# Kernel optimization log

Hardware: AMD Instinct MI355X
Metric: run time of the kernel (lower is better)

Reference implementation:

```python
import jax, jax.numpy as jnp
import numpy as np

B = 1024      # molecules (segments)
K = 16        # conformers per molecule
N = B * K     # total nodes
C = 128       # in_out_dimension
HID = 256     # hidden_dimension of gate MLP
HEADS = 2
LAYERS = 2


def _leaky(x, slope):
    return jnp.where(x >= 0, x, slope * x)


def setup_inputs() -> dict:
    key = jax.random.key(0)
    ks = jax.random.split(key, 12)
    # segment ids: K conformers per molecule, sorted
    batch = jnp.repeat(jnp.arange(B, dtype=jnp.int64), K)
    # fully connected within each segment, no self loops, then append self loops
    idx = np.arange(N, dtype=np.int64).reshape(B, K)
    src = np.broadcast_to(idx[:, :, None], (B, K, K)).reshape(-1)
    dst = np.broadcast_to(idx[:, None, :], (B, K, K)).reshape(-1)
    keep = src != dst
    e_src = jnp.asarray(np.concatenate([src[keep], np.arange(N, dtype=np.int64)]))
    e_dst = jnp.asarray(np.concatenate([dst[keep], np.arange(N, dtype=np.int64)]))
    sc = 1.0 / np.sqrt(C)
    sh = 1.0 / np.sqrt(HID)
    inp = {
        "H": jax.random.normal(ks[0], (N, C), jnp.float32),
        "batch": batch,
        "edge_src": e_src,
        "edge_dst": e_dst,
        "Wl": jax.random.normal(ks[1], (LAYERS, C, HEADS * C), jnp.float32) * sc,
        "bl": jnp.zeros((LAYERS, HEADS * C), jnp.float32),
        "Wr": jax.random.normal(ks[2], (LAYERS, C, HEADS * C), jnp.float32) * sc,
        "br": jnp.zeros((LAYERS, HEADS * C), jnp.float32),
        "att": jax.random.normal(ks[3], (LAYERS, HEADS, C), jnp.float32) * sc,
        "gat_bias": jnp.zeros((LAYERS, C), jnp.float32),
        "gW1": jax.random.normal(ks[4], (C, HID), jnp.float32) * sc,
        "gb1": jnp.zeros((HID,), jnp.float32),
        "gW2": jax.random.normal(ks[5], (HID, HID), jnp.float32) * sh,
        "gb2": jnp.zeros((HID,), jnp.float32),
        "gW3": jax.random.normal(ks[6], (HID, 1), jnp.float32) * sh,
        "gb3": jnp.zeros((1,), jnp.float32),
    }
    return inp


def _segment_softmax(logits, seg, num_segments):
    m = jax.ops.segment_max(logits, seg, num_segments=num_segments)
    ex = jnp.exp(logits - m[seg])
    den = jax.ops.segment_sum(ex, seg, num_segments=num_segments)
    return ex / den[seg]


def _gatv2(x, e_src, e_dst, Wl, bl, Wr, br, att, bias):
    # GATv2Conv, concat=False (mean over heads), negative_slope=0.2
    xl = (x @ Wl + bl).reshape(N, HEADS, C)   # source transform
    xr = (x @ Wr + br).reshape(N, HEADS, C)   # target transform
    e = _leaky(xl[e_src] + xr[e_dst], 0.2)    # [E, H, C]
    logits = jnp.einsum('ehc,hc->eh', e, att) # [E, H]
    alpha = _segment_softmax(logits, e_dst, N)
    out = jax.ops.segment_sum(xl[e_src] * alpha[:, :, None], e_dst, num_segments=N)
    return out.mean(axis=1) + bias            # [N, C]


def reference(H, batch, edge_src, edge_dst, Wl, bl, Wr, br, att, gat_bias,
              gW1, gb1, gW2, gb2, gW3, gb3):
    x = H
    for l in range(LAYERS):
        x = _gatv2(x, edge_src, edge_dst, Wl[l], bl[l], Wr[l], br[l], att[l], gat_bias[l])
    # gate MLP (LeakyReLU default slope 0.01)
    h = _leaky(x @ gW1 + gb1, 0.01)
    h = _leaky(h @ gW2 + gb2, 0.01)
    h_gate = h @ gW3 + gb3                    # [N, 1]
    scores = _segment_softmax(h_gate, batch, B)
    h_pool = jax.ops.segment_sum(x * scores, batch, num_segments=B)  # [B, C]
    return (h_pool, scores)
```

## Files before the change

kernel.cpp:

```cpp
#include <hip/hip_runtime.h>
#include <hip/hip_bf16.h>
#include <math.h>

#define N_NODES 16384
#define B_MOL   1024

typedef __attribute__((ext_vector_type(8))) short short8v;
typedef __attribute__((ext_vector_type(4))) float f32x4;

static __device__ __forceinline__ unsigned short f2bf(float f) {
    unsigned int u = __float_as_uint(f);
    unsigned int r = (u + 0x7FFFu + ((u >> 16) & 1u)) >> 16;
    return (unsigned short)r;
}
static __device__ __forceinline__ float bf2f(unsigned short h) {
    return __uint_as_float(((unsigned int)h) << 16);
}

__global__ __launch_bounds__(256)
void conv_pack(const float* __restrict__ Wl, const float* __restrict__ Wr,
               const float* __restrict__ g1, const float* __restrict__ g2,
               unsigned short* __restrict__ wpk) {
    int idx = blockIdx.x * 256 + threadIdx.x;
    if (idx >= 229376) return;
    float v; size_t base; int nK, k, col;
    if (idx < 131072) {
        int l = idx >> 16;
        int e = idx & 65535;
        k = e >> 9; col = e & 511;
        v = (col < 256) ? Wl[l * 32768 + k * 256 + col]
                        : Wr[l * 32768 + k * 256 + (col - 256)];
        base = (size_t)l * 131072; nK = 4;
    } else if (idx < 163840) {
        int e = idx - 131072; k = e >> 8; col = e & 255;
        v = g1[k * 256 + col]; base = 262144; nK = 4;
    } else {
        int e = idx - 163840; k = e >> 8; col = e & 255;
        v = g2[k * 256 + col]; base = 327680; nK = 8;
    }
    int cb = col >> 4, ci = col & 15, ks = k >> 5, kk = k & 31;
    int lane = ((kk >> 3) << 4) | ci;
    size_t fo = ((size_t)(cb * nK + ks) * 2) * 512 + lane * 8 + (kk & 7);
    unsigned short h = f2bf(v);
    wpk[base + fo] = h;
    wpk[base + fo + 512] = f2bf(v - bf2f(h));
}

template<int NK, int NCB>
static __device__ __forceinline__ void tile_gemm(
        const short* __restrict__ Ah, const short* __restrict__ Al,
        const unsigned short* __restrict__ wv,
        f32x4 (&acc)[2][NCB], int lane) {
    int lr = lane & 15;
    int kq = (lane >> 4) * 8;
    short8v bc[NCB][2], bn[NCB][2];
    #pragma unroll
    for (int j = 0; j < NCB; ++j) {
        bc[j][0] = *(const short8v*)&wv[((j * NK + 0) * 2 + 0) * 512 + lane * 8];
        bc[j][1] = *(const short8v*)&wv[((j * NK + 0) * 2 + 1) * 512 + lane * 8];
    }
    #pragma unroll
    for (int ks = 0; ks < NK; ++ks) {
        if (ks + 1 < NK) {
            #pragma unroll
            for (int j = 0; j < NCB; ++j) {
                bn[j][0] = *(const short8v*)&wv[((j * NK + ks + 1) * 2 + 0) * 512 + lane * 8];
                bn[j][1] = *(const short8v*)&wv[((j * NK + ks + 1) * 2 + 1) * 512 + lane * 8];
            }
        }
        short8v ah[2], al[2];
        #pragma unroll
        for (int i = 0; i < 2; ++i) {
            int ro = (i * 16 + lr) * 264 + ks * 32 + kq;
            ah[i] = *(const short8v*)&Ah[ro];
            al[i] = *(const short8v*)&Al[ro];
        }
        #pragma unroll
        for (int i = 0; i < 2; ++i)
            #pragma unroll
            for (int j = 0; j < NCB; ++j) {
                acc[i][j] = __builtin_amdgcn_mfma_f32_16x16x32_bf16(ah[i], bc[j][0], acc[i][j], 0, 0, 0);
                acc[i][j] = __builtin_amdgcn_mfma_f32_16x16x32_bf16(ah[i], bc[j][1], acc[i][j], 0, 0, 0);
                acc[i][j] = __builtin_amdgcn_mfma_f32_16x16x32_bf16(al[i], bc[j][0], acc[i][j], 0, 0, 0);
            }
        if (ks + 1 < NK) {
            #pragma unroll
            for (int j = 0; j < NCB; ++j) { bc[j][0] = bn[j][0]; bc[j][1] = bn[j][1]; }
        }
    }
}

static __device__ __forceinline__ void pack_pair(f32x4 o, short4* ph, short4* pl) {
    unsigned short h0 = f2bf(o[0]), h1 = f2bf(o[1]), h2 = f2bf(o[2]), h3 = f2bf(o[3]);
    *ph = make_short4((short)h0, (short)h1, (short)h2, (short)h3);
    *pl = make_short4((short)f2bf(o[0] - bf2f(h0)), (short)f2bf(o[1] - bf2f(h1)),
                      (short)f2bf(o[2] - bf2f(h2)), (short)f2bf(o[3] - bf2f(h3)));
}

__global__ __launch_bounds__(512, 1)
void mega(const float* __restrict__ H, const unsigned short* __restrict__ wpk,
          const float* __restrict__ bl, const float* __restrict__ br,
          const float* __restrict__ att, const float* __restrict__ gbias,
          const float* __restrict__ gb1, const float* __restrict__ gb2,
          const float* __restrict__ gW3, const float* __restrict__ gb3,
          float* __restrict__ out) {
    __shared__ short sAh[32][264], sAl[32][264];
    __shared__ float sL[32][260], sR[32][260];
    __shared__ float sXf[32][132];
    __shared__ float sLog[2][32][20];
    __shared__ float sg[32], ssc[32];

    int tid  = threadIdx.x;
    int lane = tid & 63;
    int w    = tid >> 6;
    int lr   = lane & 15;
    int rowBase = blockIdx.x * 32;

    {
        int r = tid >> 4, q = tid & 15;
        const float* hp = H + (size_t)(rowBase + r) * 128 + q * 8;
        #pragma unroll
        for (int u = 0; u < 2; ++u) {
            f32x4 v = *(const f32x4*)&hp[u * 4];
            pack_pair(v, (short4*)&sAh[r][q * 8 + u * 4], (short4*)&sAl[r][q * 8 + u * 4]);
        }
    }
    __syncthreads();

    for (int l = 0; l < 2; ++l) {
        {
            f32x4 acc[2][4];
            #pragma unroll
            for (int i = 0; i < 2; ++i)
                #pragma unroll
                for (int j = 0; j < 4; ++j) acc[i][j] = (f32x4){0.f, 0.f, 0.f, 0.f};
            tile_gemm<4, 4>(&sAh[0][0], &sAl[0][0],
                            wpk + (size_t)l * 131072 + (size_t)w * 16384, acc, lane);
            float* dst; int cbase; const float* bp;
            if (w < 4) { dst = &sL[0][0]; cbase = w * 64; bp = bl + l * 256 + w * 64; }
            else       { dst = &sR[0][0]; cbase = (w - 4) * 64; bp = br + l * 256 + (w - 4) * 64; }
            #pragma unroll
            for (int i = 0; i < 2; ++i) {
                int row0 = i * 16 + (lane >> 4) * 4;
                #pragma unroll
                for (int j = 0; j < 4; ++j) {
                    int cl = j * 16 + lr;
                    float bv = bp[cl];
                    #pragma unroll
                    for (int t = 0; t < 4; ++t)
                        dst[(row0 + t) * 260 + cbase + cl] = acc[i][j][t] + bv;
                }
            }
        }
        __syncthreads();

        {
            int m2l = tid >> 8;
            int r8  = tid & 255;
            int hh  = r8 >> 7;
            int db  = (r8 >> 5) & 3;
            int sb  = (r8 >> 3) & 3;
            int cq  = r8 & 7;
            float ac[4][4];
            #pragma unroll
            for (int di = 0; di < 4; ++di)
                #pragma unroll
                for (int si = 0; si < 4; ++si) ac[di][si] = 0.f;
            #pragma unroll
            for (int t = 0; t < 4; ++t) {
                int c4 = cq + 8 * t;
                f32x4 av = *(const f32x4*)&att[l * 256 + hh * 128 + c4 * 4];
                f32x4 a6 = av * 0.6f, a4 = av * 0.4f;
                f32x4 xrv[4], xlv[4];
                #pragma unroll
                for (int di = 0; di < 4; ++di)
                    xrv[di] = *(const f32x4*)&sR[m2l * 16 + db * 4 + di][hh * 128 + c4 * 4];
                #pragma unroll
                for (int si = 0; si < 4; ++si)
                    xlv[si] = *(const f32x4*)&sL[m2l * 16 + sb * 4 + si][hh * 128 + c4 * 4];
                #pragma unroll
                for (int di = 0; di < 4; ++di)
                    #pragma unroll
                    for (int si = 0; si < 4; ++si) {
                        f32x4 e = xlv[si] + xrv[di];
                        ac[di][si] += a6[0] * e[0] + a4[0] * fabsf(e[0])
                                    + a6[1] * e[1] + a4[1] * fabsf(e[1])
                                    + a6[2] * e[2] + a4[2] * fabsf(e[2])
                                    + a6[3] * e[3] + a4[3] * fabsf(e[3]);
                    }
            }
            #pragma unroll
            for (int di = 0; di < 4; ++di)
                #pragma unroll
                for (int si = 0; si < 4; ++si) {
                    float v = ac[di][si];
                    v += __shfl_down(v, 4);
                    v += __shfl_down(v, 2);
                    v += __shfl_down(v, 1);
                    if (cq == 0)
                        sLog[m2l][(db * 4 + di) * 2 + hh][sb * 4 + si] = v;
                }
        }
        __syncthreads();

        if (tid < 64) {
            int ms = tid >> 5, dhs = tid & 31;
            float vb[16], mx = -1e30f;
            #pragma unroll
            for (int s = 0; s < 16; ++s) { vb[s] = sLog[ms][dhs][s]; mx = fmaxf(mx, vb[s]); }
            float den = 0.f;
            #pragma unroll
            for (int s = 0; s < 16; ++s) { vb[s] = expf(vb[s] - mx); den += vb[s]; }
            float inv = 1.f / den;
            #pragma unroll
            for (int s = 0; s < 16; ++s) sLog[ms][dhs][s] = vb[s] * inv;
        }
        __syncthreads();

        {
            int m2a = tid >> 8;
            int d  = (tid >> 4) & 15;
            int cw = tid & 15;
            f32x4 f0 = (f32x4){0.f, 0.f, 0.f, 0.f};
            f32x4 f1 = (f32x4){0.f, 0.f, 0.f, 0.f};
            #pragma unroll
            for (int hh = 0; hh < 2; ++hh) {
                const float* alr = &sLog[m2a][d * 2 + hh][0];
                #pragma unroll
                for (int s = 0; s < 16; ++s) {
                    int se = (s + cw) & 15;
                    float al = alr[se];
                    const float* xp = &sL[m2a * 16 + se][hh * 128 + cw * 8];
                    f0 += al * *(const f32x4*)xp;
                    f1 += al * *(const f32x4*)(xp + 4);
                }
            }
            f32x4 o0 = f0 * 0.5f + *(const f32x4*)&gbias[l * 128 + cw * 8];
            f32x4 o1 = f1 * 0.5f + *(const f32x4*)&gbias[l * 128 + cw * 8 + 4];
            int row = m2a * 16 + d;
            pack_pair(o0, (short4*)&sAh[row][cw * 8],     (short4*)&sAl[row][cw * 8]);
            pack_pair(o1, (short4*)&sAh[row][cw * 8 + 4], (short4*)&sAl[row][cw * 8 + 4]);
            if (l == 1) {
                *(f32x4*)&sXf[row][cw * 8]     = o0;
                *(f32x4*)&sXf[row][cw * 8 + 4] = o1;
            }
        }
        __syncthreads();
    }

    {
        f32x4 acc[2][2];
        #pragma unroll
        for (int i = 0; i < 2; ++i)
            #pragma unroll
            for (int j = 0; j < 2; ++j) acc[i][j] = (f32x4){0.f, 0.f, 0.f, 0.f};
        tile_gemm<4, 2>(&sAh[0][0], &sAl[0][0],
                        wpk + 262144 + (size_t)w * 8192, acc, lane);
        __syncthreads();
        #pragma unroll
        for (int i = 0; i < 2; ++i) {
            int row0 = i * 16 + (lane >> 4) * 4;
            #pragma unroll
            for (int j = 0; j < 2; ++j) {
                int cl = w * 32 + j * 16 + lr;
                float bv = gb1[cl];
                #pragma unroll
                for (int t = 0; t < 4; ++t) {
                    float v = acc[i][j][t] + bv;
                    v = v >= 0.f ? v : 0.01f * v;
                    unsigned short h = f2bf(v);
                    sAh[row0 + t][cl] = (short)h;
                    sAl[row0 + t][cl] = (short)f2bf(v - bf2f(h));
                }
            }
        }
    }
    __syncthreads();

    {
        f32x4 acc[2][2];
        #pragma unroll
        for (int i = 0; i < 2; ++i)
            #pragma unroll
            for (int j = 0; j < 2; ++j) acc[i][j] = (f32x4){0.f, 0.f, 0.f, 0.f};
        tile_gemm<8, 2>(&sAh[0][0], &sAl[0][0],
                        wpk + 327680 + (size_t)w * 16384, acc, lane);
        #pragma unroll
        for (int i = 0; i < 2; ++i) {
            int row0 = i * 16 + (lane >> 4) * 4;
            #pragma unroll
            for (int j = 0; j < 2; ++j) {
                int cl = w * 32 + j * 16 + lr;
                float bv = gb2[cl];
                #pragma unroll
                for (int t = 0; t < 4; ++t) {
                    float v = acc[i][j][t] + bv;
                    v = v >= 0.f ? v : 0.01f * v;
                    sR[row0 + t][cl] = v;
                }
            }
        }
    }
    __syncthreads();

    {
        int grow = tid >> 4, l16 = tid & 15;
        float p = 0.f;
        #pragma unroll
        for (int u = 0; u < 4; ++u) {
            f32x4 h2v = *(const f32x4*)&sR[grow][l16 * 16 + u * 4];
            f32x4 w3v = *(const f32x4*)&gW3[l16 * 16 + u * 4];
            p += h2v[0] * w3v[0] + h2v[1] * w3v[1] + h2v[2] * w3v[2] + h2v[3] * w3v[3];
        }
        p += __shfl_down(p, 8);
        p += __shfl_down(p, 4);
        p += __shfl_down(p, 2);
        p += __shfl_down(p, 1);
        if (l16 == 0) sg[grow] = p + gb3[0];
    }
    __syncthreads();

    if (tid < 32) {
        float v = sg[tid];
        float mx = v;
        #pragma unroll
        for (int off = 8; off; off >>= 1) mx = fmaxf(mx, __shfl_xor(mx, off, 16));
        float e = expf(v - mx);
        float den = e;
        #pragma unroll
        for (int off = 8; off; off >>= 1) den += __shfl_xor(den, off, 16);
        float sc = e / den;
        ssc[tid] = sc;
        out[131072 + rowBase + tid] = sc;
    }
    __syncthreads();

    if (tid < 256) {
        int cc = tid & 127;
        int mp = tid >> 7;
        float a = 0.f;
        #pragma unroll
        for (int s = 0; s < 16; ++s)
            a += ssc[mp * 16 + s] * sXf[mp * 16 + s][cc];
        out[(size_t)(blockIdx.x * 2 + mp) * 128 + cc] = a;
    }
}

extern "C" void kernel_launch(void* const* d_in, const int* in_sizes, int n_in,
                              void* d_out, int out_size, void* d_ws, size_t ws_size,
                              hipStream_t stream) {
    (void)in_sizes; (void)n_in; (void)out_size; (void)ws_size;
    const float* H        = (const float*)d_in[0];
    const float* Wl       = (const float*)d_in[4];
    const float* bl       = (const float*)d_in[5];
    const float* Wr       = (const float*)d_in[6];
    const float* br       = (const float*)d_in[7];
    const float* att      = (const float*)d_in[8];
    const float* gat_bias = (const float*)d_in[9];
    const float* gW1      = (const float*)d_in[10];
    const float* gb1      = (const float*)d_in[11];
    const float* gW2      = (const float*)d_in[12];
    const float* gb2      = (const float*)d_in[13];
    const float* gW3      = (const float*)d_in[14];
    const float* gb3      = (const float*)d_in[15];
    float* out = (float*)d_out;

    unsigned short* wpk = (unsigned short*)d_ws;

    conv_pack<<<896, 256, 0, stream>>>(Wl, Wr, gW1, gW2, wpk);
    mega<<<512, 512, 0, stream>>>(H, wpk, bl, br, att, gat_bias,
                                  gb1, gb2, gW3, gb3, out);
}
```

Before: 65.89 us.

## Remap mega kernel to one molecule per 256-thread block

Each block now handles a single 16-node molecule with 4 waves instead of two molecules with 8 waves, doubling the grid to 1024 blocks. Shared memory is roughly halved and launch bounds target 3 blocks per CU, so more blocks can be resident and overlap their barrier-separated phases. The GEMM helper now works on one 16-row tile with MFMAs grouped by weight fragment, and each wave covers twice the output columns. The trade-off is that weights are read from global memory by twice as many blocks, and each block does less work per barrier.

```diff
diff --git a/kernel.cpp b/kernel.cpp
--- a/kernel.cpp
+++ b/kernel.cpp
@@ -47,10 +47,10 @@
 }
 
 template<int NK, int NCB>
-static __device__ __forceinline__ void tile_gemm(
+static __device__ __forceinline__ void tile_gemm16(
         const short* __restrict__ Ah, const short* __restrict__ Al,
         const unsigned short* __restrict__ wv,
-        f32x4 (&acc)[2][NCB], int lane) {
+        f32x4 (&acc)[NCB], int lane) {
     int lr = lane & 15;
     int kq = (lane >> 4) * 8;
     short8v bc[NCB][2], bn[NCB][2];
@@ -68,21 +68,18 @@
                 bn[j][1] = *(const short8v*)&wv[((j * NK + ks + 1) * 2 + 1) * 512 + lane * 8];
             }
         }
-        short8v ah[2], al[2];
-        #pragma unroll
-        for (int i = 0; i < 2; ++i) {
-            int ro = (i * 16 + lr) * 264 + ks * 32 + kq;
-            ah[i] = *(const short8v*)&Ah[ro];
-            al[i] = *(const short8v*)&Al[ro];
-        }
-        #pragma unroll
-        for (int i = 0; i < 2; ++i)
-            #pragma unroll
-            for (int j = 0; j < NCB; ++j) {
-                acc[i][j] = __builtin_amdgcn_mfma_f32_16x16x32_bf16(ah[i], bc[j][0], acc[i][j], 0, 0, 0);
-                acc[i][j] = __builtin_amdgcn_mfma_f32_16x16x32_bf16(ah[i], bc[j][1], acc[i][j], 0, 0, 0);
-                acc[i][j] = __builtin_amdgcn_mfma_f32_16x16x32_bf16(al[i], bc[j][0], acc[i][j], 0, 0, 0);
-            }
+        int ro = lr * 264 + ks * 32 + kq;
+        short8v ah = *(const short8v*)&Ah[ro];
+        short8v al = *(const short8v*)&Al[ro];
+        #pragma unroll
+        for (int j = 0; j < NCB; ++j)
+            acc[j] = __builtin_amdgcn_mfma_f32_16x16x32_bf16(ah, bc[j][0], acc[j], 0, 0, 0);
+        #pragma unroll
+        for (int j = 0; j < NCB; ++j)
+            acc[j] = __builtin_amdgcn_mfma_f32_16x16x32_bf16(ah, bc[j][1], acc[j], 0, 0, 0);
+        #pragma unroll
+        for (int j = 0; j < NCB; ++j)
+            acc[j] = __builtin_amdgcn_mfma_f32_16x16x32_bf16(al, bc[j][0], acc[j], 0, 0, 0);
         if (ks + 1 < NK) {
             #pragma unroll
             for (int j = 0; j < NCB; ++j) { bc[j][0] = bn[j][0]; bc[j][1] = bn[j][1]; }
@@ -97,24 +94,24 @@
                       (short)f2bf(o[2] - bf2f(h2)), (short)f2bf(o[3] - bf2f(h3)));
 }
 
-__global__ __launch_bounds__(512, 1)
+__global__ __launch_bounds__(256, 3)
 void mega(const float* __restrict__ H, const unsigned short* __restrict__ wpk,
           const float* __restrict__ bl, const float* __restrict__ br,
           const float* __restrict__ att, const float* __restrict__ gbias,
           const float* __restrict__ gb1, const float* __restrict__ gb2,
           const float* __restrict__ gW3, const float* __restrict__ gb3,
           float* __restrict__ out) {
-    __shared__ short sAh[32][264], sAl[32][264];
-    __shared__ float sL[32][260], sR[32][260];
-    __shared__ float sXf[32][132];
-    __shared__ float sLog[2][32][20];
-    __shared__ float sg[32], ssc[32];
+    __shared__ short sAh[16][264], sAl[16][264];
+    __shared__ float sL[16][260], sR[16][260];
+    __shared__ float sLog[32][20];
+    __shared__ float sg[16], ssc[16];
 
     int tid  = threadIdx.x;
     int lane = tid & 63;
     int w    = tid >> 6;
     int lr   = lane & 15;
-    int rowBase = blockIdx.x * 32;
+    int mol  = blockIdx.x;
+    int rowBase = mol * 16;
 
     {
         int r = tid >> 4, q = tid & 15;
@@ -128,39 +125,34 @@
     __syncthreads();
 
     for (int l = 0; l < 2; ++l) {
+        #pragma unroll
+        for (int c = 0; c < 2; ++c) {
+            f32x4 acc[4];
+            #pragma unroll
+            for (int j = 0; j < 4; ++j) acc[j] = (f32x4){0.f, 0.f, 0.f, 0.f};
+            tile_gemm16<4, 4>(&sAh[0][0], &sAl[0][0],
+                              wpk + (size_t)l * 131072 + ((size_t)w * 8 + c * 4) * 4096,
+                              acc, lane);
+            float* dst; int cbase; const float* bp;
+            if (w < 2) { dst = &sL[0][0]; cbase = w * 128 + c * 64; bp = bl + l * 256; }
+            else       { dst = &sR[0][0]; cbase = (w - 2) * 128 + c * 64; bp = br + l * 256; }
+            int row0 = (lane >> 4) * 4;
+            #pragma unroll
+            for (int j = 0; j < 4; ++j) {
+                int cl = cbase + j * 16 + lr;
+                float bv = bp[cl];
+                #pragma unroll
+                for (int t = 0; t < 4; ++t)
+                    dst[(row0 + t) * 260 + cl] = acc[j][t] + bv;
+            }
+        }
+        __syncthreads();
+
         {
-            f32x4 acc[2][4];
-            #pragma unroll
-            for (int i = 0; i < 2; ++i)
-                #pragma unroll
-                for (int j = 0; j < 4; ++j) acc[i][j] = (f32x4){0.f, 0.f, 0.f, 0.f};
-            tile_gemm<4, 4>(&sAh[0][0], &sAl[0][0],
-                            wpk + (size_t)l * 131072 + (size_t)w * 16384, acc, lane);
-            float* dst; int cbase; const float* bp;
-            if (w < 4) { dst = &sL[0][0]; cbase = w * 64; bp = bl + l * 256 + w * 64; }
-            else       { dst = &sR[0][0]; cbase = (w - 4) * 64; bp = br + l * 256 + (w - 4) * 64; }
-            #pragma unroll
-            for (int i = 0; i < 2; ++i) {
-                int row0 = i * 16 + (lane >> 4) * 4;
-                #pragma unroll
-                for (int j = 0; j < 4; ++j) {
-                    int cl = j * 16 + lr;
-                    float bv = bp[cl];
-                    #pragma unroll
-                    for (int t = 0; t < 4; ++t)
-                        dst[(row0 + t) * 260 + cbase + cl] = acc[i][j][t] + bv;
-                }
-            }
-        }
-        __syncthreads();
-
-        {
-            int m2l = tid >> 8;
-            int r8  = tid & 255;
-            int hh  = r8 >> 7;
-            int db  = (r8 >> 5) & 3;
-            int sb  = (r8 >> 3) & 3;
-            int cq  = r8 & 7;
+            int hh  = tid >> 7;
+            int db  = (tid >> 5) & 3;
+            int sb  = (tid >> 3) & 3;
+            int cq  = tid & 7;
             float ac[4][4];
             #pragma unroll
             for (int di = 0; di < 4; ++di)
@@ -174,10 +166,10 @@
                 f32x4 xrv[4], xlv[4];
                 #pragma unroll
                 for (int di = 0; di < 4; ++di)
-                    xrv[di] = *(const f32x4*)&sR[m2l * 16 + db * 4 + di][hh * 128 + c4 * 4];
+                    xrv[di] = *(const f32x4*)&sR[db * 4 + di][hh * 128 + c4 * 4];
                 #pragma unroll
                 for (int si = 0; si < 4; ++si)
-                    xlv[si] = *(const f32x4*)&sL[m2l * 16 + sb * 4 + si][hh * 128 + c4 * 4];
+                    xlv[si] = *(const f32x4*)&sL[sb * 4 + si][hh * 128 + c4 * 4];
                 #pragma unroll
                 for (int di = 0; di < 4; ++di)
                     #pragma unroll
@@ -198,106 +190,93 @@
                     v += __shfl_down(v, 2);
                     v += __shfl_down(v, 1);
                     if (cq == 0)
-                        sLog[m2l][(db * 4 + di) * 2 + hh][sb * 4 + si] = v;
+                        sLog[(db * 4 + di) * 2 + hh][sb * 4 + si] = v;
                 }
         }
         __syncthreads();
 
-        if (tid < 64) {
-            int ms = tid >> 5, dhs = tid & 31;
+        if (tid < 32) {
             float vb[16], mx = -1e30f;
             #pragma unroll
-            for (int s = 0; s < 16; ++s) { vb[s] = sLog[ms][dhs][s]; mx = fmaxf(mx, vb[s]); }
+            for (int s = 0; s < 16; ++s) { vb[s] = sLog[tid][s]; mx = fmaxf(mx, vb[s]); }
             float den = 0.f;
             #pragma unroll
             for (int s = 0; s < 16; ++s) { vb[s] = expf(vb[s] - mx); den += vb[s]; }
             float inv = 1.f / den;
             #pragma unroll
-            for (int s = 0; s < 16; ++s) sLog[ms][dhs][s] = vb[s] * inv;
+            for (int s = 0; s < 16; ++s) sLog[tid][s] = vb[s] * inv;
         }
         __syncthreads();
 
         {
-            int m2a = tid >> 8;
-            int d  = (tid >> 4) & 15;
+            int d  = tid >> 4;
             int cw = tid & 15;
             f32x4 f0 = (f32x4){0.f, 0.f, 0.f, 0.f};
             f32x4 f1 = (f32x4){0.f, 0.f, 0.f, 0.f};
             #pragma unroll
             for (int hh = 0; hh < 2; ++hh) {
-                const float* alr = &sLog[m2a][d * 2 + hh][0];
+                const float* alr = &sLog[d * 2 + hh][0];
                 #pragma unroll
                 for (int s = 0; s < 16; ++s) {
                     int se = (s + cw) & 15;
                     float al = alr[se];
-                    const float* xp = &sL[m2a * 16 + se][hh * 128 + cw * 8];
+                    const float* xp = &sL[se][hh * 128 + cw * 8];
                     f0 += al * *(const f32x4*)xp;
                     f1 += al * *(const f32x4*)(xp + 4);
                 }
             }
             f32x4 o0 = f0 * 0.5f + *(const f32x4*)&gbias[l * 128 + cw * 8];
             f32x4 o1 = f1 * 0.5f + *(const f32x4*)&gbias[l * 128 + cw * 8 + 4];
-            int row = m2a * 16 + d;
-            pack_pair(o0, (short4*)&sAh[row][cw * 8],     (short4*)&sAl[row][cw * 8]);
-            pack_pair(o1, (short4*)&sAh[row][cw * 8 + 4], (short4*)&sAl[row][cw * 8 + 4]);
+            pack_pair(o0, (short4*)&sAh[d][cw * 8],     (short4*)&sAl[d][cw * 8]);
+            pack_pair(o1, (short4*)&sAh[d][cw * 8 + 4], (short4*)&sAl[d][cw * 8 + 4]);
             if (l == 1) {
-                *(f32x4*)&sXf[row][cw * 8]     = o0;
-                *(f32x4*)&sXf[row][cw * 8 + 4] = o1;
+                *(f32x4*)&sR[d][128 + cw * 8]     = o0;
+                *(f32x4*)&sR[d][128 + cw * 8 + 4] = o1;
             }
         }
         __syncthreads();
     }
 
     {
-        f32x4 acc[2][2];
-        #pragma unroll
-        for (int i = 0; i < 2; ++i)
-            #pragma unroll
-            for (int j = 0; j < 2; ++j) acc[i][j] = (f32x4){0.f, 0.f, 0.f, 0.f};
-        tile_gemm<4, 2>(&sAh[0][0], &sAl[0][0],
-                        wpk + 262144 + (size_t)w * 8192, acc, lane);
-        __syncthreads();
-        #pragma unroll
-        for (int i = 0; i < 2; ++i) {
-            int row0 = i * 16 + (lane >> 4) * 4;
-            #pragma unroll
-            for (int j = 0; j < 2; ++j) {
-                int cl = w * 32 + j * 16 + lr;
-                float bv = gb1[cl];
-                #pragma unroll
-                for (int t = 0; t < 4; ++t) {
-                    float v = acc[i][j][t] + bv;
-                    v = v >= 0.f ? v : 0.01f * v;
-                    unsigned short h = f2bf(v);
-                    sAh[row0 + t][cl] = (short)h;
-                    sAl[row0 + t][cl] = (short)f2bf(v - bf2f(h));
-                }
+        f32x4 acc[4];
+        #pragma unroll
+        for (int j = 0; j < 4; ++j) acc[j] = (f32x4){0.f, 0.f, 0.f, 0.f};
+        tile_gemm16<4, 4>(&sAh[0][0], &sAl[0][0],
+                          wpk + 262144 + (size_t)w * 16384, acc, lane);
+        __syncthreads();
+        int row0 = (lane >> 4) * 4;
+        #pragma unroll
+        for (int j = 0; j < 4; ++j) {
+            int cl = w * 64 + j * 16 + lr;
+            float bv = gb1[cl];
+            #pragma unroll
+            for (int t = 0; t < 4; ++t) {
+                float v = acc[j][t] + bv;
+                v = v >= 0.f ? v : 0.01f * v;
+                unsigned short h = f2bf(v);
+                sAh[row0 + t][cl] = (short)h;
+                sAl[row0 + t][cl] = (short)f2bf(v - bf2f(h));
             }
         }
     }
     __syncthreads();
 
     {
-        f32x4 acc[2][2];
-        #pragma unroll
-        for (int i = 0; i < 2; ++i)
-            #pragma unroll
-            for (int j = 0; j < 2; ++j) acc[i][j] = (f32x4){0.f, 0.f, 0.f, 0.f};
-        tile_gemm<8, 2>(&sAh[0][0], &sAl[0][0],
-                        wpk + 327680 + (size_t)w * 16384, acc, lane);
-        #pragma unroll
-        for (int i = 0; i < 2; ++i) {
-            int row0 = i * 16 + (lane >> 4) * 4;
-            #pragma unroll
-            for (int j = 0; j < 2; ++j) {
-                int cl = w * 32 + j * 16 + lr;
-                float bv = gb2[cl];
-                #pragma unroll
-                for (int t = 0; t < 4; ++t) {
-                    float v = acc[i][j][t] + bv;
-                    v = v >= 0.f ? v : 0.01f * v;
-                    sR[row0 + t][cl] = v;
-                }
+        f32x4 acc[4];
+        #pragma unroll
+        for (int j = 0; j < 4; ++j) acc[j] = (f32x4){0.f, 0.f, 0.f, 0.f};
+        tile_gemm16<8, 4>(&sAh[0][0], &sAl[0][0],
+                          wpk + 327680 + (size_t)w * 32768, acc, lane);
+        int row0 = (lane >> 4) * 4;
+        #pragma unroll
+        for (int j = 0; j < 4; ++j) {
+            int cl = w * 64 + j * 16 + lr;
+            float bv = gb2[cl];
+            #pragma unroll
+            for (int t = 0; t < 4; ++t) {
+                float v = acc[j][t] + bv;
+                v = v >= 0.f ? v : 0.01f * v;
+                sL[row0 + t][cl] = v;
             }
         }
     }
@@ -308,7 +287,7 @@
         float p = 0.f;
         #pragma unroll
         for (int u = 0; u < 4; ++u) {
-            f32x4 h2v = *(const f32x4*)&sR[grow][l16 * 16 + u * 4];
+            f32x4 h2v = *(const f32x4*)&sL[grow][l16 * 16 + u * 4];
             f32x4 w3v = *(const f32x4*)&gW3[l16 * 16 + u * 4];
             p += h2v[0] * w3v[0] + h2v[1] * w3v[1] + h2v[2] * w3v[2] + h2v[3] * w3v[3];
         }
@@ -320,7 +299,7 @@
     }
     __syncthreads();
 
-    if (tid < 32) {
+    if (tid < 16) {
         float v = sg[tid];
         float mx = v;
         #pragma unroll
@@ -335,14 +314,12 @@
     }
     __syncthreads();
 
-    if (tid < 256) {
-        int cc = tid & 127;
-        int mp = tid >> 7;
+    if (tid < 128) {
         float a = 0.f;
         #pragma unroll
         for (int s = 0; s < 16; ++s)
-            a += ssc[mp * 16 + s] * sXf[mp * 16 + s][cc];
-        out[(size_t)(blockIdx.x * 2 + mp) * 128 + cc] = a;
+            a += ssc[s] * sR[s][128 + tid];
+        out[(size_t)mol * 128 + tid] = a;
     }
 }
 
@@ -368,6 +345,6 @@
     unsigned short* wpk = (unsigned short*)d_ws;
 
     conv_pack<<<896, 256, 0, stream>>>(Wl, Wr, gW1, gW2, wpk);
-    mega<<<512, 512, 0, stream>>>(H, wpk, bl, br, att, gat_bias,
-                                  gb1, gb2, gW3, gb3, out);
-}
+    mega<<<B_MOL, 256, 0, stream>>>(H, wpk, bl, br, att, gat_bias,
+                                    gb1, gb2, gW3, gb3, out);
+}
```

After: 107.4 us. 62.9% more time.

## Double block threads to 1024 and split GEMM and attention work finer

Applied to the files above, without the earlier changes.

Each block now runs 1024 threads (16 waves) instead of 512 over the same 32-row tile. Each wave gets half as many column blocks in every GEMM. The attention logits are computed one (dst, head, src) pair per thread with the segment softmax fused in via shuffles, which removes a separate softmax pass and one barrier. The att vector is staged in shared memory, and the sXf buffer is dropped by reusing sR. This raises in-block parallelism and latency hiding, but each wave does less MFMA work per weight load and register pressure per thread is capped tighter.

```diff
diff --git a/kernel.cpp b/kernel.cpp
--- a/kernel.cpp
+++ b/kernel.cpp
@@ -47,7 +47,7 @@
 }
 
 template<int NK, int NCB>
-static __device__ __forceinline__ void tile_gemm(
+static __device__ __forceinline__ void tile_gemm32(
         const short* __restrict__ Ah, const short* __restrict__ Al,
         const unsigned short* __restrict__ wv,
         f32x4 (&acc)[2][NCB], int lane) {
@@ -97,7 +97,7 @@
                       (short)f2bf(o[2] - bf2f(h2)), (short)f2bf(o[3] - bf2f(h3)));
 }
 
-__global__ __launch_bounds__(512, 1)
+__global__ __launch_bounds__(1024)
 void mega(const float* __restrict__ H, const unsigned short* __restrict__ wpk,
           const float* __restrict__ bl, const float* __restrict__ br,
           const float* __restrict__ att, const float* __restrict__ gbias,
@@ -106,8 +106,8 @@
           float* __restrict__ out) {
     __shared__ short sAh[32][264], sAl[32][264];
     __shared__ float sL[32][260], sR[32][260];
-    __shared__ float sXf[32][132];
     __shared__ float sLog[2][32][20];
+    __shared__ float sAtt[512];
     __shared__ float sg[32], ssc[32];
 
     int tid  = threadIdx.x;
@@ -117,206 +117,154 @@
     int rowBase = blockIdx.x * 32;
 
     {
-        int r = tid >> 4, q = tid & 15;
-        const float* hp = H + (size_t)(rowBase + r) * 128 + q * 8;
-        #pragma unroll
-        for (int u = 0; u < 2; ++u) {
-            f32x4 v = *(const f32x4*)&hp[u * 4];
-            pack_pair(v, (short4*)&sAh[r][q * 8 + u * 4], (short4*)&sAl[r][q * 8 + u * 4]);
-        }
+        int r = tid >> 5, q = tid & 31;
+        f32x4 v = *(const f32x4*)&H[(size_t)(rowBase + r) * 128 + q * 4];
+        pack_pair(v, (short4*)&sAh[r][q * 4], (short4*)&sAl[r][q * 4]);
+        if (tid < 512) sAtt[tid] = att[tid];
     }
     __syncthreads();
 
     for (int l = 0; l < 2; ++l) {
         {
-            f32x4 acc[2][4];
+            f32x4 acc[2][2];
             #pragma unroll
             for (int i = 0; i < 2; ++i)
                 #pragma unroll
-                for (int j = 0; j < 4; ++j) acc[i][j] = (f32x4){0.f, 0.f, 0.f, 0.f};
-            tile_gemm<4, 4>(&sAh[0][0], &sAl[0][0],
-                            wpk + (size_t)l * 131072 + (size_t)w * 16384, acc, lane);
+                for (int j = 0; j < 2; ++j) acc[i][j] = (f32x4){0.f, 0.f, 0.f, 0.f};
+            tile_gemm32<4, 2>(&sAh[0][0], &sAl[0][0],
+                              wpk + (size_t)l * 131072 + (size_t)w * 8192, acc, lane);
             float* dst; int cbase; const float* bp;
-            if (w < 4) { dst = &sL[0][0]; cbase = w * 64; bp = bl + l * 256 + w * 64; }
-            else       { dst = &sR[0][0]; cbase = (w - 4) * 64; bp = br + l * 256 + (w - 4) * 64; }
+            if (w < 8) { dst = &sL[0][0]; cbase = w * 32; bp = bl + l * 256; }
+            else       { dst = &sR[0][0]; cbase = (w - 8) * 32; bp = br + l * 256; }
             #pragma unroll
             for (int i = 0; i < 2; ++i) {
                 int row0 = i * 16 + (lane >> 4) * 4;
                 #pragma unroll
-                for (int j = 0; j < 4; ++j) {
-                    int cl = j * 16 + lr;
+                for (int j = 0; j < 2; ++j) {
+                    int cl = cbase + j * 16 + lr;
                     float bv = bp[cl];
                     #pragma unroll
                     for (int t = 0; t < 4; ++t)
-                        dst[(row0 + t) * 260 + cbase + cl] = acc[i][j][t] + bv;
+                        dst[(row0 + t) * 260 + cl] = acc[i][j][t] + bv;
                 }
             }
         }
         __syncthreads();
 
         {
-            int m2l = tid >> 8;
-            int r8  = tid & 255;
-            int hh  = r8 >> 7;
-            int db  = (r8 >> 5) & 3;
-            int sb  = (r8 >> 3) & 3;
-            int cq  = r8 & 7;
-            float ac[4][4];
-            #pragma unroll
-            for (int di = 0; di < 4; ++di)
-                #pragma unroll
-                for (int si = 0; si < 4; ++si) ac[di][si] = 0.f;
-            #pragma unroll
-            for (int t = 0; t < 4; ++t) {
-                int c4 = cq + 8 * t;
-                f32x4 av = *(const f32x4*)&att[l * 256 + hh * 128 + c4 * 4];
-                f32x4 a6 = av * 0.6f, a4 = av * 0.4f;
-                f32x4 xrv[4], xlv[4];
-                #pragma unroll
-                for (int di = 0; di < 4; ++di)
-                    xrv[di] = *(const f32x4*)&sR[m2l * 16 + db * 4 + di][hh * 128 + c4 * 4];
-                #pragma unroll
-                for (int si = 0; si < 4; ++si)
-                    xlv[si] = *(const f32x4*)&sL[m2l * 16 + sb * 4 + si][hh * 128 + c4 * 4];
-                #pragma unroll
-                for (int di = 0; di < 4; ++di)
-                    #pragma unroll
-                    for (int si = 0; si < 4; ++si) {
-                        f32x4 e = xlv[si] + xrv[di];
-                        ac[di][si] += a6[0] * e[0] + a4[0] * fabsf(e[0])
-                                    + a6[1] * e[1] + a4[1] * fabsf(e[1])
-                                    + a6[2] * e[2] + a4[2] * fabsf(e[2])
-                                    + a6[3] * e[3] + a4[3] * fabsf(e[3]);
-                    }
-            }
-            #pragma unroll
-            for (int di = 0; di < 4; ++di)
-                #pragma unroll
-                for (int si = 0; si < 4; ++si) {
-                    float v = ac[di][si];
-                    v += __shfl_down(v, 4);
-                    v += __shfl_down(v, 2);
-                    v += __shfl_down(v, 1);
-                    if (cq == 0)
-                        sLog[m2l][(db * 4 + di) * 2 + hh][sb * 4 + si] = v;
-                }
+            int m2l = tid >> 9;
+            int rem = tid & 511;
+            int dh  = rem >> 4;
+            int s   = rem & 15;
+            int d   = dh >> 1, hh = dh & 1;
+            const float* xrp = &sR[m2l * 16 + d][hh * 128];
+            const float* xlp = &sL[m2l * 16 + s][hh * 128];
+            const float* ap  = &sAtt[l * 256 + hh * 128];
+            float ac = 0.f;
+            #pragma unroll 8
+            for (int c4 = 0; c4 < 32; ++c4) {
+                f32x4 av = *(const f32x4*)&ap[c4 * 4];
+                f32x4 xv = *(const f32x4*)&xlp[c4 * 4];
+                f32x4 rv = *(const f32x4*)&xrp[c4 * 4];
+                f32x4 e = xv + rv;
+                ac += 0.6f * av[0] * e[0] + 0.4f * av[0] * fabsf(e[0])
+                    + 0.6f * av[1] * e[1] + 0.4f * av[1] * fabsf(e[1])
+                    + 0.6f * av[2] * e[2] + 0.4f * av[2] * fabsf(e[2])
+                    + 0.6f * av[3] * e[3] + 0.4f * av[3] * fabsf(e[3]);
+            }
+            float mx = ac;
+            #pragma unroll
+            for (int off = 1; off < 16; off <<= 1)
+                mx = fmaxf(mx, __shfl_xor(mx, off, 16));
+            float e = expf(ac - mx);
+            float den = e;
+            #pragma unroll
+            for (int off = 1; off < 16; off <<= 1)
+                den += __shfl_xor(den, off, 16);
+            sLog[m2l][dh][s] = e / den;
         }
         __syncthreads();
 
-        if (tid < 64) {
-            int ms = tid >> 5, dhs = tid & 31;
-            float vb[16], mx = -1e30f;
-            #pragma unroll
-            for (int s = 0; s < 16; ++s) { vb[s] = sLog[ms][dhs][s]; mx = fmaxf(mx, vb[s]); }
-            float den = 0.f;
-            #pragma unroll
-            for (int s = 0; s < 16; ++s) { vb[s] = expf(vb[s] - mx); den += vb[s]; }
-            float inv = 1.f / den;
-            #pragma unroll
-            for (int s = 0; s < 16; ++s) sLog[ms][dhs][s] = vb[s] * inv;
-        }
-        __syncthreads();
-
         {
-            int m2a = tid >> 8;
-            int d  = (tid >> 4) & 15;
-            int cw = tid & 15;
+            int m2a = tid >> 9;
+            int rem = tid & 511;
+            int d  = rem >> 5;
+            int cw = rem & 31;
             f32x4 f0 = (f32x4){0.f, 0.f, 0.f, 0.f};
-            f32x4 f1 = (f32x4){0.f, 0.f, 0.f, 0.f};
             #pragma unroll
             for (int hh = 0; hh < 2; ++hh) {
                 const float* alr = &sLog[m2a][d * 2 + hh][0];
                 #pragma unroll
                 for (int s = 0; s < 16; ++s) {
                     int se = (s + cw) & 15;
-                    float al = alr[se];
-                    const float* xp = &sL[m2a * 16 + se][hh * 128 + cw * 8];
-                    f0 += al * *(const f32x4*)xp;
-                    f1 += al * *(const f32x4*)(xp + 4);
+                    f0 += alr[se] * *(const f32x4*)&sL[m2a * 16 + se][hh * 128 + cw * 4];
                 }
             }
-            f32x4 o0 = f0 * 0.5f + *(const f32x4*)&gbias[l * 128 + cw * 8];
-            f32x4 o1 = f1 * 0.5f + *(const f32x4*)&gbias[l * 128 + cw * 8 + 4];
+            f32x4 o = f0 * 0.5f + *(const f32x4*)&gbias[l * 128 + cw * 4];
             int row = m2a * 16 + d;
-            pack_pair(o0, (short4*)&sAh[row][cw * 8],     (short4*)&sAl[row][cw * 8]);
-            pack_pair(o1, (short4*)&sAh[row][cw * 8 + 4], (short4*)&sAl[row][cw * 8 + 4]);
-            if (l == 1) {
-                *(f32x4*)&sXf[row][cw * 8]     = o0;
-                *(f32x4*)&sXf[row][cw * 8 + 4] = o1;
-            }
+            pack_pair(o, (short4*)&sAh[row][cw * 4], (short4*)&sAl[row][cw * 4]);
+            if (l == 1)
+                *(f32x4*)&sR[row][128 + cw * 4] = o;
         }
         __syncthreads();
     }
 
     {
-        f32x4 acc[2][2];
-        #pragma unroll
-        for (int i = 0; i < 2; ++i)
-            #pragma unroll
-            for (int j = 0; j < 2; ++j) acc[i][j] = (f32x4){0.f, 0.f, 0.f, 0.f};
-        tile_gemm<4, 2>(&sAh[0][0], &sAl[0][0],
-                        wpk + 262144 + (size_t)w * 8192, acc, lane);
+        f32x4 acc[2][1];
+        acc[0][0] = (f32x4){0.f, 0.f, 0.f, 0.f};
+        acc[1][0] = (f32x4){0.f, 0.f, 0.f, 0.f};
+        tile_gemm32<4, 1>(&sAh[0][0], &sAl[0][0],
+                          wpk + 262144 + (size_t)w * 4096, acc, lane);
         __syncthreads();
+        int cl = w * 16 + lr;
+        float bv = gb1[cl];
         #pragma unroll
         for (int i = 0; i < 2; ++i) {
             int row0 = i * 16 + (lane >> 4) * 4;
             #pragma unroll
-            for (int j = 0; j < 2; ++j) {
-                int cl = w * 32 + j * 16 + lr;
-                float bv = gb1[cl];
-                #pragma unroll
-                for (int t = 0; t < 4; ++t) {
-                    float v = acc[i][j][t] + bv;
-                    v = v >= 0.f ? v : 0.01f * v;
-                    unsigned short h = f2bf(v);
-                    sAh[row0 + t][cl] = (short)h;
-                    sAl[row0 + t][cl] = (short)f2bf(v - bf2f(h));
-                }
+            for (int t = 0; t < 4; ++t) {
+                float v = acc[i][0][t] + bv;
+                v = v >= 0.f ? v : 0.01f * v;
+                unsigned short h = f2bf(v);
+                sAh[row0 + t][cl] = (short)h;
+                sAl[row0 + t][cl] = (short)f2bf(v - bf2f(h));
             }
         }
     }
     __syncthreads();
 
     {
-        f32x4 acc[2][2];
-        #pragma unroll
-        for (int i = 0; i < 2; ++i)
-            #pragma unroll
-            for (int j = 0; j < 2; ++j) acc[i][j] = (f32x4){0.f, 0.f, 0.f, 0.f};
-        tile_gemm<8, 2>(&sAh[0][0], &sAl[0][0],
-                        wpk + 327680 + (size_t)w * 16384, acc, lane);
+        f32x4 acc[2][1];
+        acc[0][0] = (f32x4){0.f, 0.f, 0.f, 0.f};
+        acc[1][0] = (f32x4){0.f, 0.f, 0.f, 0.f};
+        tile_gemm32<8, 1>(&sAh[0][0], &sAl[0][0],
+                          wpk + 327680 + (size_t)w * 8192, acc, lane);
+        int cl = w * 16 + lr;
+        float bv = gb2[cl];
         #pragma unroll
         for (int i = 0; i < 2; ++i) {
             int row0 = i * 16 + (lane >> 4) * 4;
             #pragma unroll
-            for (int j = 0; j < 2; ++j) {
-                int cl = w * 32 + j * 16 + lr;
-                float bv = gb2[cl];
-                #pragma unroll
-                for (int t = 0; t < 4; ++t) {
-                    float v = acc[i][j][t] + bv;
-                    v = v >= 0.f ? v : 0.01f * v;
-                    sR[row0 + t][cl] = v;
-                }
-            }
-        }
-    }
-    __syncthreads();
-
-    {
-        int grow = tid >> 4, l16 = tid & 15;
-        float p = 0.f;
-        #pragma unroll
-        for (int u = 0; u < 4; ++u) {
-            f32x4 h2v = *(const f32x4*)&sR[grow][l16 * 16 + u * 4];
-            f32x4 w3v = *(const f32x4*)&gW3[l16 * 16 + u * 4];
-            p += h2v[0] * w3v[0] + h2v[1] * w3v[1] + h2v[2] * w3v[2] + h2v[3] * w3v[3];
-        }
-        p += __shfl_down(p, 8);
-        p += __shfl_down(p, 4);
-        p += __shfl_down(p, 2);
-        p += __shfl_down(p, 1);
-        if (l16 == 0) sg[grow] = p + gb3[0];
+            for (int t = 0; t < 4; ++t) {
+                float v = acc[i][0][t] + bv;
+                v = v >= 0.f ? v : 0.01f * v;
+                sL[row0 + t][cl] = v;
+            }
+        }
+    }
+    __syncthreads();
+
+    if (tid < 1024) {
+        int grow = tid >> 5, l32 = tid & 31;
+        f32x4 h2a = *(const f32x4*)&sL[grow][l32 * 8];
+        f32x4 h2b = *(const f32x4*)&sL[grow][l32 * 8 + 4];
+        f32x4 w3a = *(const f32x4*)&gW3[l32 * 8];
+        f32x4 w3b = *(const f32x4*)&gW3[l32 * 8 + 4];
+        float p = h2a[0] * w3a[0] + h2a[1] * w3a[1] + h2a[2] * w3a[2] + h2a[3] * w3a[3]
+                + h2b[0] * w3b[0] + h2b[1] * w3b[1] + h2b[2] * w3b[2] + h2b[3] * w3b[3];
+        #pragma unroll
+        for (int off = 16; off; off >>= 1) p += __shfl_down(p, off, 32);
+        if (l32 == 0) sg[grow] = p + gb3[0];
     }
     __syncthreads();
 
@@ -341,7 +289,7 @@
         float a = 0.f;
         #pragma unroll
         for (int s = 0; s < 16; ++s)
-            a += ssc[mp * 16 + s] * sXf[mp * 16 + s][cc];
+            a += ssc[mp * 16 + s] * sR[mp * 16 + s][128 + cc];
         out[(size_t)(blockIdx.x * 2 + mp) * 128 + cc] = a;
     }
 }
@@ -368,6 +316,6 @@
     unsigned short* wpk = (unsigned short*)d_ws;
 
     conv_pack<<<896, 256, 0, stream>>>(Wl, Wr, gW1, gW2, wpk);
-    mega<<<512, 512, 0, stream>>>(H, wpk, bl, br, att, gat_bias,
-                                  gb1, gb2, gW3, gb3, out);
-}
+    mega<<<B_MOL / 2, 1024, 0, stream>>>(H, wpk, bl, br, att, gat_bias,
+                                         gb1, gb2, gW3, gb3, out);
+}
```

Measured after the change: 76.82 us. +16.6%, slower.
